# Kernel tuning notes

Hardware: AMD Instinct MI355X
Metric: run time of the kernel (lower is better)

## Reference

```python
import jax, jax.numpy as jnp
import numpy as np


def setup_inputs() -> dict:
    key = jax.random.key(0)
    kQ, kS, kR, kP = jax.random.split(key, 4)
    B, C, Cv = 4, 128, 128
    h, w = 128, 128
    H, W = 256, 256
    k = 16
    Q = jax.random.normal(kQ, (B, C, h, w), dtype=jnp.float32)
    S = jax.random.normal(kS, (B, C, H, W), dtype=jnp.float32)
    R = jax.random.normal(kR, (B, Cv, H, W), dtype=jnp.float32)
    Pos = jax.random.randint(kP, (B, 2, h, w, k), 0, 256, dtype=jnp.int32)
    return {"Q": Q, "S": S, "R": R, "Pos": Pos}


def reference(Q, S, R, Pos):
    # Q: (B, C, h, w); S: (B, C, H, W); R: (B, Cv, H, W); Pos: (B, 2, h, w, k)
    B, C, h, w = Q.shape
    _, Cv, H, W = R.shape
    k = Pos.shape[-1]
    hw = h * w

    # Flatten (x, y) neighbor coords into linear indices over H*W: (B, hw*k)
    flat_idx = (Pos[:, 0].reshape(B, -1).astype(jnp.int32) * W
                + Pos[:, 1].reshape(B, -1).astype(jnp.int32))

    # Gather epipolar neighborhoods (vectorized over batch, no python loop)
    KeyG = jnp.take_along_axis(S.reshape(B, C, H * W), flat_idx[:, None, :], axis=2)
    ValG = jnp.take_along_axis(R.reshape(B, Cv, H * W), flat_idx[:, None, :], axis=2)
    Key = KeyG.reshape(B, C, hw, k)    # (B, C, hw, k)
    Val = ValG.reshape(B, Cv, hw, k)   # (B, Cv, hw, k)

    Qr = Q.transpose(0, 2, 3, 1).reshape(B, hw, C)          # (B, hw, C)
    score = jnp.einsum('bpc,bcpk->bpk', Qr, Key)            # (B, hw, k)
    attn = jax.nn.softmax(score, axis=-1)                   # (B, hw, k)
    out = jnp.einsum('bpk,bcpk->bpc', attn, Val)            # (B, hw, Cv)

    buffer = out.reshape(B, h, w, Cv).transpose(0, 3, 1, 2)  # (B, Cv, h, w)
    M_right_to_left = attn[:, :, None, :]                    # (B, hw, 1, k) as in torch
    return buffer, M_right_to_left
```

## Files before the change

### kernel.cpp

```cpp
#include <hip/hip_runtime.h>

constexpr int B  = 4;
constexpr int C  = 128;
constexpr int hw = 16384;
constexpr int W_ = 256;
constexpr int HW = 65536;
constexpr int K  = 16;
constexpr int P_TILE = 16;
constexpr int BLOCKS_PER_BATCH = hw / P_TILE;

typedef __attribute__((ext_vector_type(4))) _Float16 half4v;
typedef __attribute__((ext_vector_type(8))) _Float16 half8;

__global__ __launch_bounds__(256) void transpose_kv_f16(
    const float* __restrict__ S, const float* __restrict__ R,
    _Float16* __restrict__ KV)
{
    __shared__ _Float16 kv[256 * 128];
    const int z   = blockIdx.z;
    const int n0  = blockIdx.x * 128;
    const int tid = threadIdx.x;
    const int n4  = tid & 31;
    const int rg  = tid >> 5;

    const float* s = S + (size_t)z * C * HW;
    const float* r = R + (size_t)z * C * HW;

    #pragma unroll
    for (int i = 0; i < 16; ++i) {
        const int cl = rg + 8 * i;
        const float4 vs = *reinterpret_cast<const float4*>(
            &s[(size_t)cl * HW + n0 + 4 * n4]);
        const float4 vr = *reinterpret_cast<const float4*>(
            &r[(size_t)cl * HW + n0 + 4 * n4]);
        const int chS = cl;
        const int chR = cl + 128;
        const int npS = n4 ^ ((chS >> 3) & 31);
        const int npR = n4 ^ ((chR >> 3) & 31);
        half4v hs, hr;
        hs[0] = (_Float16)vs.x; hs[1] = (_Float16)vs.y;
        hs[2] = (_Float16)vs.z; hs[3] = (_Float16)vs.w;
        hr[0] = (_Float16)vr.x; hr[1] = (_Float16)vr.y;
        hr[2] = (_Float16)vr.z; hr[3] = (_Float16)vr.w;
        *reinterpret_cast<half4v*>(&kv[chS * 128 + 4 * npS]) = hs;
        *reinterpret_cast<half4v*>(&kv[chR * 128 + 4 * npR]) = hr;
    }
    __syncthreads();

    _Float16* dbase = KV + (size_t)z * HW * 256;
    const int u  = tid & 31;
    const int rl = tid >> 5;
    #pragma unroll
    for (int p = 0; p < 16; ++p) {
        const int nn = rl + 8 * p;
        const int q  = nn >> 2;
        const int rm = nn & 3;
        half8 hv;
        #pragma unroll
        for (int i = 0; i < 8; ++i) {
            const int ch = 8 * u + i;
            hv[i] = kv[ch * 128 + ((q ^ u) << 2) + rm];
        }
        *reinterpret_cast<half8*>(&dbase[(size_t)(n0 + nn) * 256 + 8 * u]) = hv;
    }
}

__global__ __launch_bounds__(256) void attn_gather_kv(
    const float* __restrict__ Q, const int* __restrict__ Pos,
    const _Float16* __restrict__ KV,
    float* __restrict__ outBuf, float* __restrict__ outM, int b0)
{
    __shared__ float q_s[P_TILE][132];
    __shared__ float out_s[P_TILE][132];

    const int tid = threadIdx.x;
    const int bb  = blockIdx.x / BLOCKS_PER_BATCH;
    const int b   = b0 + bb;
    const int p0  = (blockIdx.x % BLOCKS_PER_BATCH) * P_TILE;

    for (int i = tid; i < P_TILE * C; i += 256) {
        int c = i >> 4, pl0 = i & 15;
        q_s[pl0][c] = Q[((size_t)(b * C + c)) * hw + p0 + pl0];
    }
    const int pl = tid >> 4;
    const int cg = tid & 15;
    const int p  = p0 + pl;
    int myidx;
    {
        const int rr = Pos[(((size_t)(b * 2 + 0) * hw) + p) * K + cg];
        const int cc = Pos[(((size_t)(b * 2 + 1) * hw) + p) * K + cg];
        myidx = rr * W_ + cc;
    }
    __syncthreads();

    float qf[8];
    #pragma unroll
    for (int i = 0; i < 8; ++i) qf[i] = q_s[pl][cg * 8 + i];

    float m = -1e30f, l = 0.f, myscore = 0.f;
    float acc[8];
    #pragma unroll
    for (int i = 0; i < 8; ++i) acc[i] = 0.f;

    const half8* base = reinterpret_cast<const half8*>(KV) + (size_t)bb * HW * 32;

    #pragma unroll
    for (int kc = 0; kc < K; kc += 8) {
        half8 kreg[8], vreg[8];
        #pragma unroll
        for (int r = 0; r < 8; ++r) {
            const int ridx = __shfl(myidx, kc + r, 16);
            const half8* row = base + (size_t)ridx * 32;
            kreg[r] = row[cg];
            vreg[r] = row[16 + cg];
        }
        #pragma unroll
        for (int r = 0; r < 8; ++r) {
            float part = 0.f;
            #pragma unroll
            for (int i = 0; i < 8; ++i) part += qf[i] * (float)kreg[r][i];
            #pragma unroll
            for (int off = 1; off < 16; off <<= 1) part += __shfl_xor(part, off);
            const float mn    = fmaxf(m, part);
            const float scale = __expf(m - mn);
            const float e     = __expf(part - mn);
            l = l * scale + e;
            #pragma unroll
            for (int i = 0; i < 8; ++i) acc[i] = acc[i] * scale + e * (float)vreg[r][i];
            m = mn;
            if (cg == kc + r) myscore = part;
        }
    }

    const float inv_l = 1.0f / l;
    const float attn  = __expf(myscore - m) * inv_l;
    outM[((size_t)b * hw + p) * K + cg] = attn;
    #pragma unroll
    for (int i = 0; i < 8; ++i) out_s[pl][cg * 8 + i] = acc[i] * inv_l;
    __syncthreads();
    for (int i = tid; i < P_TILE * C; i += 256) {
        int c = i >> 4, pl3 = i & 15;
        outBuf[((size_t)(b * C + c)) * hw + p0 + pl3] = out_s[pl3][c];
    }
}

__global__ __launch_bounds__(256) void attn_direct(
    const float* __restrict__ Q, const float* __restrict__ S, const float* __restrict__ R,
    const int* __restrict__ Pos, float* __restrict__ outBuf, float* __restrict__ outM)
{
    __shared__ float q_s[P_TILE][132];
    __shared__ float attn_s[P_TILE][17];
    __shared__ int   idx_s[P_TILE][K];
    __shared__ float out_s[P_TILE][132];

    const int tid = threadIdx.x;
    const int b   = blockIdx.x / BLOCKS_PER_BATCH;
    const int p0  = (blockIdx.x % BLOCKS_PER_BATCH) * P_TILE;

    for (int i = tid; i < P_TILE * C; i += 256) {
        int c = i >> 4, pl0 = i & 15;
        q_s[pl0][c] = Q[((size_t)(b * C + c)) * hw + p0 + pl0];
    }
    const int pl = tid >> 4;
    const int kk = tid & 15;
    const int p  = p0 + pl;
    const int rr = Pos[(((size_t)(b * 2 + 0) * hw) + p) * K + kk];
    const int cc = Pos[(((size_t)(b * 2 + 1) * hw) + p) * K + kk];
    const int idx = rr * W_ + cc;
    idx_s[pl][kk] = idx;
    __syncthreads();

    float score = 0.f;
    {
        const float* srow = S + (size_t)b * C * HW + idx;
        for (int c = 0; c < C; ++c) score += q_s[pl][c] * srow[(size_t)c * HW];
    }
    float mx = score;
    #pragma unroll
    for (int off = 1; off < 16; off <<= 1) mx = fmaxf(mx, __shfl_xor(mx, off));
    float e = __expf(score - mx);
    float ssum = e;
    #pragma unroll
    for (int off = 1; off < 16; off <<= 1) ssum += __shfl_xor(ssum, off);
    const float attn = e / ssum;
    outM[((size_t)b * hw + p) * K + kk] = attn;
    attn_s[pl][kk] = attn;
    __syncthreads();

    {
        const int pl2 = tid >> 4;
        const int cg  = tid & 15;
        float acc[8];
        #pragma unroll
        for (int i = 0; i < 8; ++i) acc[i] = 0.f;
        for (int k2 = 0; k2 < K; ++k2) {
            const float a = attn_s[pl2][k2];
            const float* rw = R + (size_t)b * C * HW + idx_s[pl2][k2];
            #pragma unroll
            for (int i = 0; i < 8; ++i) acc[i] += a * rw[(size_t)(cg * 8 + i) * HW];
        }
        #pragma unroll
        for (int i = 0; i < 8; ++i) out_s[pl2][cg * 8 + i] = acc[i];
    }
    __syncthreads();
    for (int i = tid; i < P_TILE * C; i += 256) {
        int c = i >> 4, pl3 = i & 15;
        outBuf[((size_t)(b * C + c)) * hw + p0 + pl3] = out_s[pl3][c];
    }
}

extern "C" void kernel_launch(void* const* d_in, const int* in_sizes, int n_in,
                              void* d_out, int out_size, void* d_ws, size_t ws_size,
                              hipStream_t stream)
{
    (void)in_sizes; (void)n_in; (void)out_size;
    const float* Q  = (const float*)d_in[0];
    const float* S  = (const float*)d_in[1];
    const float* R  = (const float*)d_in[2];
    const int*  Pos = (const int*)d_in[3];
    float* outBuf = (float*)d_out;
    float* outM   = outBuf + (size_t)B * C * hw;

    const size_t fullBytes     = (size_t)B * HW * 256 * sizeof(_Float16);
    const size_t perBatchBytes = (size_t)HW * 256 * sizeof(_Float16);

    dim3 tb(256);
    if (ws_size >= fullBytes) {
        _Float16* KVt = (_Float16*)d_ws;
        dim3 tg(HW / 128, 1, B);
        transpose_kv_f16<<<tg, tb, 0, stream>>>(S, R, KVt);
        attn_gather_kv<<<dim3(B * BLOCKS_PER_BATCH), 256, 0, stream>>>(
            Q, Pos, KVt, outBuf, outM, 0);
    } else if (ws_size >= perBatchBytes) {
        _Float16* KVt = (_Float16*)d_ws;
        dim3 tg(HW / 128, 1, 1);
        for (int b = 0; b < B; ++b) {
            transpose_kv_f16<<<tg, tb, 0, stream>>>(
                S + (size_t)b * C * HW, R + (size_t)b * C * HW, KVt);
            attn_gather_kv<<<dim3(BLOCKS_PER_BATCH), 256, 0, stream>>>(
                Q, Pos, KVt, outBuf, outM, b);
        }
    } else {
        attn_direct<<<dim3(B * BLOCKS_PER_BATCH), 256, 0, stream>>>(
            Q, S, R, Pos, outBuf, outM);
    }
}
```

Measured before the change: 397.4 us.

## Make transpose kernel persistent over four tiles with register prefetch of next tile

```diff
diff --git a/kernel.cpp b/kernel.cpp
--- a/kernel.cpp
+++ b/kernel.cpp
@@ -17,51 +17,66 @@
     _Float16* __restrict__ KV)
 {
     __shared__ _Float16 kv[256 * 128];
-    const int z   = blockIdx.z;
-    const int n0  = blockIdx.x * 128;
     const int tid = threadIdx.x;
     const int n4  = tid & 31;
     const int rg  = tid >> 5;
-
-    const float* s = S + (size_t)z * C * HW;
-    const float* r = R + (size_t)z * C * HW;
-
-    #pragma unroll
-    for (int i = 0; i < 16; ++i) {
-        const int cl = rg + 8 * i;
-        const float4 vs = *reinterpret_cast<const float4*>(
-            &s[(size_t)cl * HW + n0 + 4 * n4]);
-        const float4 vr = *reinterpret_cast<const float4*>(
-            &r[(size_t)cl * HW + n0 + 4 * n4]);
-        const int chS = cl;
-        const int chR = cl + 128;
-        const int npS = n4 ^ ((chS >> 3) & 31);
-        const int npR = n4 ^ ((chR >> 3) & 31);
-        half4v hs, hr;
-        hs[0] = (_Float16)vs.x; hs[1] = (_Float16)vs.y;
-        hs[2] = (_Float16)vs.z; hs[3] = (_Float16)vs.w;
-        hr[0] = (_Float16)vr.x; hr[1] = (_Float16)vr.y;
-        hr[2] = (_Float16)vr.z; hr[3] = (_Float16)vr.w;
-        *reinterpret_cast<half4v*>(&kv[chS * 128 + 4 * npS]) = hs;
-        *reinterpret_cast<half4v*>(&kv[chR * 128 + 4 * npR]) = hr;
-    }
-    __syncthreads();
-
-    _Float16* dbase = KV + (size_t)z * HW * 256;
-    const int u  = tid & 31;
-    const int rl = tid >> 5;
-    #pragma unroll
-    for (int p = 0; p < 16; ++p) {
-        const int nn = rl + 8 * p;
-        const int q  = nn >> 2;
-        const int rm = nn & 3;
-        half8 hv;
-        #pragma unroll
-        for (int i = 0; i < 8; ++i) {
-            const int ch = 8 * u + i;
-            hv[i] = kv[ch * 128 + ((q ^ u) << 2) + rm];
-        }
-        *reinterpret_cast<half8*>(&dbase[(size_t)(n0 + nn) * 256 + 8 * u]) = hv;
+    const int u   = tid & 31;
+    const int rl  = tid >> 5;
+
+    float4 bS[16], bR[16];
+    const int g0 = blockIdx.x * 4;
+
+    auto LOAD = [&](int gi) {
+        const int z  = gi >> 9;
+        const int n0 = (gi & 511) << 7;
+        const float* s = S + (size_t)z * C * HW + n0 + 4 * n4;
+        const float* r = R + (size_t)z * C * HW + n0 + 4 * n4;
+        #pragma unroll
+        for (int i = 0; i < 16; ++i) {
+            const int cl = rg + 8 * i;
+            bS[i] = *reinterpret_cast<const float4*>(&s[(size_t)cl * HW]);
+            bR[i] = *reinterpret_cast<const float4*>(&r[(size_t)cl * HW]);
+        }
+    };
+
+    LOAD(g0);
+    #pragma unroll
+    for (int it = 0; it < 4; ++it) {
+        __syncthreads();
+        #pragma unroll
+        for (int i = 0; i < 16; ++i) {
+            const int cl  = rg + 8 * i;
+            const int npS = n4 ^ i;
+            const int npR = n4 ^ (i + 16);
+            half4v hs, hr;
+            hs[0] = (_Float16)bS[i].x; hs[1] = (_Float16)bS[i].y;
+            hs[2] = (_Float16)bS[i].z; hs[3] = (_Float16)bS[i].w;
+            hr[0] = (_Float16)bR[i].x; hr[1] = (_Float16)bR[i].y;
+            hr[2] = (_Float16)bR[i].z; hr[3] = (_Float16)bR[i].w;
+            *reinterpret_cast<half4v*>(&kv[cl * 128 + 4 * npS])         = hs;
+            *reinterpret_cast<half4v*>(&kv[(cl + 128) * 128 + 4 * npR]) = hr;
+        }
+        if (it < 3) LOAD(g0 + it + 1);
+        __syncthreads();
+        {
+            const int gi = g0 + it;
+            const int z  = gi >> 9;
+            const int n0 = (gi & 511) << 7;
+            _Float16* dbase = KV + (size_t)z * HW * 256;
+            #pragma unroll
+            for (int p = 0; p < 16; ++p) {
+                const int nn = rl + 8 * p;
+                const int q  = nn >> 2;
+                const int rm = nn & 3;
+                half8 hv;
+                #pragma unroll
+                for (int i = 0; i < 8; ++i) {
+                    const int ch = 8 * u + i;
+                    hv[i] = kv[ch * 128 + ((q ^ u) << 2) + rm];
+                }
+                *reinterpret_cast<half8*>(&dbase[(size_t)(n0 + nn) * 256 + 8 * u]) = hv;
+            }
+        }
     }
 }
 
@@ -227,15 +242,13 @@
     dim3 tb(256);
     if (ws_size >= fullBytes) {
         _Float16* KVt = (_Float16*)d_ws;
-        dim3 tg(HW / 128, 1, B);
-        transpose_kv_f16<<<tg, tb, 0, stream>>>(S, R, KVt);
+        transpose_kv_f16<<<dim3(B * (HW / 128) / 4), tb, 0, stream>>>(S, R, KVt);
         attn_gather_kv<<<dim3(B * BLOCKS_PER_BATCH), 256, 0, stream>>>(
             Q, Pos, KVt, outBuf, outM, 0);
     } else if (ws_size >= perBatchBytes) {
         _Float16* KVt = (_Float16*)d_ws;
-        dim3 tg(HW / 128, 1, 1);
         for (int b = 0; b < B; ++b) {
-            transpose_kv_f16<<<tg, tb, 0, stream>>>(
+            transpose_kv_f16<<<dim3((HW / 128) / 4), tb, 0, stream>>>(
                 S + (size_t)b * C * HW, R + (size_t)b * C * HW, KVt);
             attn_gather_kv<<<dim3(BLOCKS_PER_BATCH), 256, 0, stream>>>(
                 Q, Pos, KVt, outBuf, outM, b);
```

Measured after the change: 398.3 us. No clear change (+0.2%).
